# Optimization experiments

Hardware: AMD Instinct MI355X
Metric: run time of the kernel (lower is better)

The kernel has to match this reference:

```python
import jax, jax.numpy as jnp
import numpy as np

B, N_NUC, N_UP, N_DOWN = 512, 16, 32, 32
N_ELEC = N_UP + N_DOWN            # 64 electrons
F = 8                             # edge feature dim (Gaussian RBF envelopes)
D = N_NUC * F                     # embedding_dim = 128 (positional electron embeddings)
L = 3                             # n_interactions
N_ATOM_TYPES = 4


def _rbf(diff):
    # diff: [..., 3] -> [..., F]; Gaussian RBF features of the interparticle distance
    d = jnp.sqrt(jnp.sum(diff * diff, axis=-1) + 1e-12)
    mu = jnp.linspace(0.0, 4.0, F, dtype=diff.dtype)
    return jnp.exp(-(d[..., None] - mu) ** 2)


def setup_inputs() -> dict:
    key = jax.random.key(0)
    ks = jax.random.split(key, 9)
    r = 2.0 * jax.random.normal(ks[0], (B, N_ELEC, 3), dtype=jnp.float32)
    R = 2.0 * jax.random.normal(ks[1], (B, N_NUC, 3), dtype=jnp.float32)
    atom_types = jax.random.randint(ks[2], (N_NUC,), 0, N_ATOM_TYPES)
    embed_table = 0.1 * jax.random.normal(ks[3], (N_ATOM_TYPES, D), dtype=jnp.float32)
    we_same = 0.1 * jax.random.normal(ks[4], (L, F, D), dtype=jnp.float32)
    we_anti = 0.1 * jax.random.normal(ks[5], (L, F, D), dtype=jnp.float32)
    we_ne = 0.1 * jax.random.normal(ks[6], (L, F, D), dtype=jnp.float32)
    w_up = 0.05 * jax.random.normal(ks[7], (L, 4 * D, D), dtype=jnp.float32)
    b_up = jnp.zeros((L, D), dtype=jnp.float32)
    return {
        'r': r, 'R': R, 'embed_table': embed_table,
        'we_same': we_same, 'we_anti': we_anti, 'we_ne': we_ne,
        'w_up': w_up, 'b_up': b_up, 'atom_types': atom_types,
    }


def reference(r, R, embed_table, we_same, we_anti, we_ne, w_up, b_up, atom_types):
    # --- molecular graph edge construction (pairwise differences + edge features) ---
    ee_feat = _rbf(r[:, :, None, :] - r[:, None, :, :])   # [B, e, e, F]
    ne_feat = _rbf(r[:, :, None, :] - R[:, None, :, :])   # [B, e, n, F]

    spin = jnp.arange(N_ELEC) >= N_UP
    eye = jnp.eye(N_ELEC, dtype=bool)
    same_m = ((spin[:, None] == spin[None, :]) & ~eye).astype(ee_feat.dtype)  # no self-interaction
    anti_m = (spin[:, None] != spin[None, :]).astype(ee_feat.dtype)
    feat_same = ee_feat * same_m[None, :, :, None]
    feat_anti = ee_feat * anti_m[None, :, :, None]

    # --- node factory: positional electron embeddings (dense scatter of ne features == reshape) ---
    x = ne_feat.reshape(ne_feat.shape[0], N_ELEC, N_NUC * F)  # [B, e, D]
    y = embed_table[atom_types]                               # [n, D] nuclei embeddings

    # --- message-passing layers ---
    for l in range(L):
        # messages = Linear(edge_feats) * sender embedding, summed over senders per receiver;
        # contract sender axis first to keep intermediates at [B, e, F, D]
        t_s = jnp.einsum('bijf,bjd->bifd', feat_same, x)
        z_s = jnp.einsum('bifd,fd->bid', t_s, we_same[l])
        t_a = jnp.einsum('bijf,bjd->bifd', feat_anti, x)
        z_a = jnp.einsum('bifd,fd->bid', t_a, we_anti[l])
        t_n = jnp.einsum('binf,nd->bifd', ne_feat, y)
        z_n = jnp.einsum('bifd,fd->bid', t_n, we_ne[l])
        upd = jnp.concatenate([x, z_s, z_a, z_n], axis=-1)    # [B, e, 4D]
        x = x + jnp.tanh(upd @ w_up[l] + b_up[l])
    return x  # final electron embeddings [B, N_ELEC, D]
```

## Files before the change

kernel.cpp:

```cpp
#include <hip/hip_runtime.h>


typedef unsigned short u16;
typedef unsigned int u32;
typedef __attribute__((ext_vector_type(8))) short short8;
typedef __attribute__((ext_vector_type(4))) float f32x4;
typedef __attribute__((ext_vector_type(4))) u32 u32x4;
typedef _Float16 h2 __attribute__((ext_vector_type(2)));

__device__ __forceinline__ u16 f2h(float f){ return __builtin_bit_cast(u16, (_Float16)f); }
__device__ __forceinline__ float h2f(u16 a){ return (float)__builtin_bit_cast(_Float16, a); }

__device__ __forceinline__ short8 rbf8(float dd){
  short8 a;
#pragma unroll
  for (int f = 0; f < 8; f++){
    float u = dd - (4.0f/7.0f)*(float)f;
    a[f] = (short)f2h(__expf(-u*u));
  }
  return a;
}

__global__ __launch_bounds__(256) void gnn_prep(
    const float* __restrict__ w_up, const float* __restrict__ we_ne,
    const float* __restrict__ embed, const int* __restrict__ atypes,
    u16* __restrict__ wsegs){
  __shared__ u16 lw[16384];
  const int blk = blockIdx.x;
  const int l = blk / 5, seg = blk % 5;
  const int tid = threadIdx.x;
  if (seg < 4){
    const float* src = w_up + (l*512 + seg*128)*128;
#pragma unroll
    for (int mm = 0; mm < 16; mm++){
      int idx = mm*1024 + tid*4;
      float4 v = *(const float4*)(src + idx);
      lw[idx+0] = f2h(v.x); lw[idx+1] = f2h(v.y);
      lw[idx+2] = f2h(v.z); lw[idx+3] = f2h(v.w);
    }
  } else {
#pragma unroll
    for (int mm = 0; mm < 16; mm++){
      int idx = mm*1024 + tid*4;
      int k = idx >> 7, dout = idx & 127;
      int n = k >> 3, f = k & 7;
      float4 ye = *(const float4*)(embed + atypes[n]*128 + dout);
      float4 wn = *(const float4*)(we_ne + (l*8 + f)*128 + dout);
      lw[idx+0] = f2h(ye.x*wn.x); lw[idx+1] = f2h(ye.y*wn.y);
      lw[idx+2] = f2h(ye.z*wn.z); lw[idx+3] = f2h(ye.w*wn.w);
    }
  }
  __syncthreads();
  u16* dst = wsegs + blk*16384;
  const int col = tid & 15, q = (tid >> 4) & 3;
#pragma unroll
  for (int m = 0; m < 8; m++){
    int slot = m*4 + (tid >> 6);
    int c = slot >> 3, nt = slot & 7;
    int kbase = c*32 + q*8;
    int dout = nt*16 + col;
    short8 vv;
#pragma unroll
    for (int jj = 0; jj < 8; jj++) vv[jj] = (short)lw[(kbase+jj)*128 + dout];
    *(short8*)(dst + m*2048 + tid*8) = vv;
  }
}

__global__ __launch_bounds__(512, 2) void gnn_main(
    const float* __restrict__ r_g, const float* __restrict__ R_g,
    const float* __restrict__ weS_g, const float* __restrict__ weA_g,
    const float* __restrict__ bup_g,
    const u16* __restrict__ wsegs,
    float* __restrict__ out)
{
  extern __shared__ __attribute__((aligned(16))) u16 lds[];
  u16* const wb0 = lds;
  u16* const wb1 = lds + 16384;
  u16* const xbB = lds + 32768;
  u16* const zsB = lds + 50176;

  const int tid  = threadIdx.x;
  const int lane = tid & 63;
  const int w    = tid >> 6;
  const int bb   = w >> 2;
  const int wq   = w & 3;
  const int b    = blockIdx.x*2 + bb;
  const int col  = lane & 15;
  const int q    = lane >> 4;
  const int i0   = wq * 16;
  const int sp   = wq >> 1;
  const int mrow = i0 + col;
  const int loff = (q*16 + col) * 8;

  u16* const xb  = xbB + bb*8704;
  u16* const zst = zsB + bb*8704;

  u32x4 stg[4];
  auto stg_ld = [&](const u16* src){
#pragma unroll
    for (int m = 0; m < 4; m++) stg[m] = *(const u32x4*)(src + m*4096 + tid*8);
  };
  auto stg_st = [&](u16* dst){
#pragma unroll
    for (int m = 0; m < 4; m++) *(u32x4*)(dst + m*4096 + tid*8) = stg[m];
  };
  auto gemm_seg = [&](const u16* wbuf, const u16* arows, f32x4* acc){
#pragma unroll
    for (int c = 0; c < 4; c++){
      short8 a = *(const short8*)(arows + mrow*136 + c*32 + (q<<3));
#pragma unroll
      for (int nt = 0; nt < 8; nt++){
        short8 bf = *(const short8*)(wbuf + c*4096 + nt*512 + loff);
        acc[nt] = __builtin_amdgcn_mfma_f32_16x16x32_f16(a, bf, acc[nt], 0, 0, 0);
      }
    }
  };

  short8 aS[8], aA[8];
  float dN[4];
  {
    float* rs = (float*)(zsB + bb*8704);
    float* Rs = rs + 256;
    const int ht = tid & 255;
    if (ht < 64){
#pragma unroll
      for (int k = 0; k < 3; k++) rs[ht*4+k] = r_g[(b*64+ht)*3 + k];
    } else if (ht < 80){
      int n = ht - 64;
#pragma unroll
      for (int k = 0; k < 3; k++) Rs[n*4+k] = R_g[(b*16+n)*3 + k];
    }
    __syncthreads();
    {
      float x0 = rs[mrow*4], x1 = rs[mrow*4+1], x2 = rs[mrow*4+2];
#pragma unroll
      for (int c = 0; c < 8; c++){
        int j = 32*sp + 4*c + q;
        float dx = x0-rs[j*4], dy = x1-rs[j*4+1], dz = x2-rs[j*4+2];
        float dd = sqrtf(dx*dx + dy*dy + dz*dz + 1e-12f);
        aS[c] = rbf8(dd);
        if (j == mrow) aS[c] = (short8)0;
        j = 32*(1-sp) + 4*c + q;
        dx = x0-rs[j*4]; dy = x1-rs[j*4+1]; dz = x2-rs[j*4+2];
        aA[c] = rbf8(sqrtf(dx*dx + dy*dy + dz*dz + 1e-12f));
      }
#pragma unroll
      for (int c = 0; c < 4; c++){
        int n = 4*c + q;
        float dx = x0-Rs[n*4], dy = x1-Rs[n*4+1], dz = x2-Rs[n*4+2];
        dN[c] = sqrtf(dx*dx + dy*dy + dz*dz + 1e-12f);
      }
    }
    {
      int i = (tid & 255) >> 2, nb = (tid & 3)*4;
      float y0 = rs[i*4], y1 = rs[i*4+1], y2 = rs[i*4+2];
#pragma unroll
      for (int nn = 0; nn < 4; nn++){
        int n = nb + nn;
        float dx = y0-Rs[n*4], dy = y1-Rs[n*4+1], dz = y2-Rs[n*4+2];
        float dd = sqrtf(dx*dx + dy*dy + dz*dz + 1e-12f);
        *(short8*)&xb[i*136 + n*8] = rbf8(dd);
      }
    }
    stg_ld(wsegs + 0);
    stg_st(wb0);
    __syncthreads();
  }

  f32x4 xr[8];
#pragma unroll
  for (int nt = 0; nt < 8; nt++)
#pragma unroll
    for (int rr = 0; rr < 4; rr++)
      xr[nt][rr] = h2f(xb[(i0 + q*4 + rr)*136 + nt*16 + col]);

  const f32x4 vzero = {0.f, 0.f, 0.f, 0.f};

#pragma unroll 1
  for (int l = 0; l < 3; l++){
    const u16* slab = wsegs + l*81920;
    const int P = l & 1;
    u16* const bufA = P ? wb1 : wb0;
    u16* const bufB = P ? wb0 : wb1;

    float bupr[8];
#pragma unroll
    for (int nt = 0; nt < 8; nt++) bupr[nt] = bup_g[l*128 + nt*16 + col];

    f32x4 upd[8];
#pragma unroll
    for (int nt = 0; nt < 8; nt++) upd[nt] = vzero;

    auto zpass = [&](int pass){
      const float* weX = pass ? weA_g : weS_g;
      const int jb0 = pass ? 32*(1-sp) : 32*sp;
      const short8* aF = pass ? aA : aS;
      f32x4 zacc[8];
#pragma unroll
      for (int nt = 0; nt < 8; nt++) zacc[nt] = vzero;
#pragma unroll
      for (int nt = 0; nt < 8; nt++){
        h2 wp[4];
#pragma unroll
        for (int p = 0; p < 4; p++){
          h2 t;
          t[0] = (_Float16)weX[(l*8 + 2*p  )*128 + nt*16 + col];
          t[1] = (_Float16)weX[(l*8 + 2*p+1)*128 + nt*16 + col];
          wp[p] = t;
        }
        u16 xv[8];
#pragma unroll
        for (int c = 0; c < 8; c++) xv[c] = xb[(jb0 + 4*c + q)*136 + nt*16 + col];
#pragma unroll
        for (int c = 0; c < 8; c++){
          _Float16 xh = __builtin_bit_cast(_Float16, xv[c]);
          h2 xd; xd[0] = xh; xd[1] = xh;
          u32x4 bu;
#pragma unroll
          for (int p = 0; p < 4; p++)
            bu[p] = __builtin_bit_cast(u32, (h2)(xd * wp[p]));
          short8 bf = __builtin_bit_cast(short8, bu);
          zacc[nt] = __builtin_amdgcn_mfma_f32_16x16x32_f16(aF[c], bf, zacc[nt], 0, 0, 0);
        }
      }
#pragma unroll
      for (int nt = 0; nt < 8; nt++)
#pragma unroll
        for (int rr = 0; rr < 4; rr++)
          zst[(i0 + q*4 + rr)*136 + nt*16 + col] = f2h(zacc[nt][rr]);
    };

    stg_ld(slab + 1*16384);
    zpass(0);
    gemm_seg(bufA, xb, upd);
    stg_st(bufB); __syncthreads();
    stg_ld(slab + 2*16384);
    gemm_seg(bufB, zst, upd);
    stg_st(bufA); __syncthreads();
    stg_ld(slab + 4*16384);
    zpass(1);
    gemm_seg(bufA, zst, upd);
    stg_st(bufB); __syncthreads();
    stg_ld(slab + 3*16384);
    {
      f32x4 zn[8];
#pragma unroll
      for (int nt = 0; nt < 8; nt++) zn[nt] = vzero;
#pragma unroll
      for (int c = 0; c < 4; c++){
        short8 a = rbf8(dN[c]);
#pragma unroll
        for (int nt = 0; nt < 8; nt++){
          short8 bf = *(const short8*)(bufB + c*4096 + nt*512 + loff);
          zn[nt] = __builtin_amdgcn_mfma_f32_16x16x32_f16(a, bf, zn[nt], 0, 0, 0);
        }
      }
#pragma unroll
      for (int nt = 0; nt < 8; nt++)
#pragma unroll
        for (int rr = 0; rr < 4; rr++)
          zst[(i0 + q*4 + rr)*136 + nt*16 + col] = f2h(zn[nt][rr]);
    }
    stg_st(bufA); __syncthreads();
    if (l < 2) stg_ld(slab + 81920);
    gemm_seg(bufA, zst, upd);
#pragma unroll
    for (int nt = 0; nt < 8; nt++){
#pragma unroll
      for (int rr = 0; rr < 4; rr++){
        float v = upd[nt][rr] + bupr[nt];
        float e = __expf(2.0f * v);
        float th = 1.0f - 2.0f * __builtin_amdgcn_rcpf(e + 1.0f);
        xr[nt][rr] += th;
      }
    }
    if (l < 2){
#pragma unroll
      for (int nt = 0; nt < 8; nt++)
#pragma unroll
        for (int rr = 0; rr < 4; rr++)
          xb[(i0 + q*4 + rr)*136 + nt*16 + col] = f2h(xr[nt][rr]);
      stg_st(bufB);
      __syncthreads();
    } else {
#pragma unroll
      for (int nt = 0; nt < 8; nt++)
#pragma unroll
        for (int rr = 0; rr < 4; rr++)
          out[(b*64 + i0 + q*4 + rr)*128 + nt*16 + col] = xr[nt][rr];
    }
  }
}

extern "C" void kernel_launch(void* const* d_in, const int* in_sizes, int n_in,
                              void* d_out, int out_size, void* d_ws, size_t ws_size,
                              hipStream_t stream){
  const float* r     = (const float*)d_in[0];
  const float* R     = (const float*)d_in[1];
  const float* embed = (const float*)d_in[2];
  const float* weS   = (const float*)d_in[3];
  const float* weA   = (const float*)d_in[4];
  const float* weN   = (const float*)d_in[5];
  const float* wup   = (const float*)d_in[6];
  const float* bup   = (const float*)d_in[7];
  const int* atyp    = (const int*)d_in[8];

  u16* wsegs = (u16*)d_ws;

  (void)hipFuncSetAttribute((const void*)gnn_main,
                            hipFuncAttributeMaxDynamicSharedMemorySize, 135168);
  gnn_prep<<<15, 256, 0, stream>>>(wup, weN, embed, atyp, wsegs);
  gnn_main<<<256, 512, 135168, stream>>>(r, R, weS, weA, bup, wsegs, (float*)d_out);
}
```

Before: 136.7 us.

## Process one batch per 256-thread block with single weight buffer

```diff
diff --git a/kernel.cpp b/kernel.cpp
--- a/kernel.cpp
+++ b/kernel.cpp
@@ -66,7 +66,7 @@
   }
 }
 
-__global__ __launch_bounds__(512, 2) void gnn_main(
+__global__ __launch_bounds__(256, 2) void gnn_main(
     const float* __restrict__ r_g, const float* __restrict__ R_g,
     const float* __restrict__ weS_g, const float* __restrict__ weA_g,
     const float* __restrict__ bup_g,
@@ -74,35 +74,29 @@
     float* __restrict__ out)
 {
   extern __shared__ __attribute__((aligned(16))) u16 lds[];
-  u16* const wb0 = lds;
-  u16* const wb1 = lds + 16384;
-  u16* const xbB = lds + 32768;
-  u16* const zsB = lds + 50176;
+  u16* const wb  = lds;
+  u16* const xb  = lds + 16384;
+  u16* const zst = lds + 25088;
 
   const int tid  = threadIdx.x;
   const int lane = tid & 63;
   const int w    = tid >> 6;
-  const int bb   = w >> 2;
-  const int wq   = w & 3;
-  const int b    = blockIdx.x*2 + bb;
+  const int b    = blockIdx.x;
   const int col  = lane & 15;
   const int q    = lane >> 4;
-  const int i0   = wq * 16;
-  const int sp   = wq >> 1;
+  const int i0   = w * 16;
+  const int sp   = w >> 1;
   const int mrow = i0 + col;
   const int loff = (q*16 + col) * 8;
 
-  u16* const xb  = xbB + bb*8704;
-  u16* const zst = zsB + bb*8704;
-
-  u32x4 stg[4];
+  u32x4 stg[8];
   auto stg_ld = [&](const u16* src){
 #pragma unroll
-    for (int m = 0; m < 4; m++) stg[m] = *(const u32x4*)(src + m*4096 + tid*8);
+    for (int m = 0; m < 8; m++) stg[m] = *(const u32x4*)(src + m*2048 + tid*8);
   };
   auto stg_st = [&](u16* dst){
 #pragma unroll
-    for (int m = 0; m < 4; m++) *(u32x4*)(dst + m*4096 + tid*8) = stg[m];
+    for (int m = 0; m < 8; m++) *(u32x4*)(dst + m*2048 + tid*8) = stg[m];
   };
   auto gemm_seg = [&](const u16* wbuf, const u16* arows, f32x4* acc){
 #pragma unroll
@@ -119,14 +113,13 @@
   short8 aS[8], aA[8];
   float dN[4];
   {
-    float* rs = (float*)(zsB + bb*8704);
+    float* rs = (float*)zst;
     float* Rs = rs + 256;
-    const int ht = tid & 255;
-    if (ht < 64){
-#pragma unroll
-      for (int k = 0; k < 3; k++) rs[ht*4+k] = r_g[(b*64+ht)*3 + k];
-    } else if (ht < 80){
-      int n = ht - 64;
+    if (tid < 64){
+#pragma unroll
+      for (int k = 0; k < 3; k++) rs[tid*4+k] = r_g[(b*64+tid)*3 + k];
+    } else if (tid < 80){
+      int n = tid - 64;
 #pragma unroll
       for (int k = 0; k < 3; k++) Rs[n*4+k] = R_g[(b*16+n)*3 + k];
     }
@@ -152,7 +145,7 @@
       }
     }
     {
-      int i = (tid & 255) >> 2, nb = (tid & 3)*4;
+      int i = tid >> 2, nb = (tid & 3)*4;
       float y0 = rs[i*4], y1 = rs[i*4+1], y2 = rs[i*4+2];
 #pragma unroll
       for (int nn = 0; nn < 4; nn++){
@@ -163,7 +156,7 @@
       }
     }
     stg_ld(wsegs + 0);
-    stg_st(wb0);
+    stg_st(wb);
     __syncthreads();
   }
 
@@ -179,9 +172,6 @@
 #pragma unroll 1
   for (int l = 0; l < 3; l++){
     const u16* slab = wsegs + l*81920;
-    const int P = l & 1;
-    u16* const bufA = P ? wb1 : wb0;
-    u16* const bufB = P ? wb0 : wb1;
 
     float bupr[8];
 #pragma unroll
@@ -232,15 +222,15 @@
 
     stg_ld(slab + 1*16384);
     zpass(0);
-    gemm_seg(bufA, xb, upd);
-    stg_st(bufB); __syncthreads();
+    gemm_seg(wb, xb, upd);
+    __syncthreads();  stg_st(wb);  __syncthreads();
     stg_ld(slab + 2*16384);
-    gemm_seg(bufB, zst, upd);
-    stg_st(bufA); __syncthreads();
+    gemm_seg(wb, zst, upd);
+    __syncthreads();  stg_st(wb);  __syncthreads();
     stg_ld(slab + 4*16384);
     zpass(1);
-    gemm_seg(bufA, zst, upd);
-    stg_st(bufB); __syncthreads();
+    gemm_seg(wb, zst, upd);
+    __syncthreads();  stg_st(wb);  __syncthreads();
     stg_ld(slab + 3*16384);
     {
       f32x4 zn[8];
@@ -251,7 +241,7 @@
         short8 a = rbf8(dN[c]);
 #pragma unroll
         for (int nt = 0; nt < 8; nt++){
-          short8 bf = *(const short8*)(bufB + c*4096 + nt*512 + loff);
+          short8 bf = *(const short8*)(wb + c*4096 + nt*512 + loff);
           zn[nt] = __builtin_amdgcn_mfma_f32_16x16x32_f16(a, bf, zn[nt], 0, 0, 0);
         }
       }
@@ -261,9 +251,9 @@
         for (int rr = 0; rr < 4; rr++)
           zst[(i0 + q*4 + rr)*136 + nt*16 + col] = f2h(zn[nt][rr]);
     }
-    stg_st(bufA); __syncthreads();
+    __syncthreads();  stg_st(wb);  __syncthreads();
     if (l < 2) stg_ld(slab + 81920);
-    gemm_seg(bufA, zst, upd);
+    gemm_seg(wb, zst, upd);
 #pragma unroll
     for (int nt = 0; nt < 8; nt++){
 #pragma unroll
@@ -280,8 +270,7 @@
 #pragma unroll
         for (int rr = 0; rr < 4; rr++)
           xb[(i0 + q*4 + rr)*136 + nt*16 + col] = f2h(xr[nt][rr]);
-      stg_st(bufB);
-      __syncthreads();
+      __syncthreads();  stg_st(wb);  __syncthreads();
     } else {
 #pragma unroll
       for (int nt = 0; nt < 8; nt++)
@@ -308,7 +297,7 @@
   u16* wsegs = (u16*)d_ws;
 
   (void)hipFuncSetAttribute((const void*)gnn_main,
-                            hipFuncAttributeMaxDynamicSharedMemorySize, 135168);
+                            hipFuncAttributeMaxDynamicSharedMemorySize, 67584);
   gnn_prep<<<15, 256, 0, stream>>>(wup, weN, embed, atyp, wsegs);
-  gnn_main<<<256, 512, 135168, stream>>>(r, R, weS, weA, bup, wsegs, (float*)d_out);
+  gnn_main<<<512, 256, 67584, stream>>>(r, R, weS, weA, bup, wsegs, (float*)d_out);
 }
```

Measured after the change: 134.5 us. About the same (-1.6%).
